# Kernel optimization log

Hardware: AMD Instinct MI355X
Metric: run time of the kernel (lower is better)

The kernel has to match this reference:

```python
import jax, jax.numpy as jnp
import numpy as np

F_, H_, W_ = 6, 16, 28          # latent video grid (frames, height, width)
DIM, NH = 1536, 12
HD = DIM // NH                   # 128
L = F_ * H_ * W_                 # 2688 tokens
EPS = 1e-6
BLOCK = 3 * H_ * W_              # block_causal_size = 3*frame_height*frame_width


def setup_inputs() -> dict:
    key = jax.random.key(0)
    ks = jax.random.split(key, 8)
    def lin(k):
        return jax.random.normal(k, (DIM, DIM), jnp.float32) * 0.02
    x = jax.random.normal(ks[0], (1, L, DIM), jnp.float32)
    # RoPE freqs: unit-modulus complex numbers stored as [...,(re,im)]
    ang = jax.random.uniform(ks[1], (1024, HD // 2), jnp.float32, -np.pi, np.pi)
    freqs = jnp.stack([jnp.cos(ang), jnp.sin(ang)], axis=-1)  # [1024, 64, 2]
    return {
        'x': x,
        'seq_lens': jnp.array([L], jnp.int32),
        'grid_sizes': jnp.array([[F_, H_, W_]], jnp.int32),
        'freqs': freqs,
        'Wq': lin(ks[2]), 'bq': jnp.zeros((DIM,), jnp.float32),
        'Wk': lin(ks[3]), 'bk': jnp.zeros((DIM,), jnp.float32),
        'Wv': lin(ks[4]), 'bv': jnp.zeros((DIM,), jnp.float32),
        'Wo': lin(ks[5]), 'bo': jnp.zeros((DIM,), jnp.float32),
        'gq': jnp.ones((DIM,), jnp.float32),
        'gk': jnp.ones((DIM,), jnp.float32),
    }


def _rmsnorm(x, g):
    # WanRMSNorm: x * rsqrt(mean(x^2) + eps) * weight
    return x * jax.lax.rsqrt(jnp.mean(x * x, axis=-1, keepdims=True) + EPS) * g


def _rope_apply(x, F, H, W, freqs, start_frame=0):
    # x: [B, L, n, d]; freqs: [1024, d//2, 2] (re, im). Per-axis split [c0, c3, c3].
    B, Lx, n, d = x.shape
    c = d // 2
    c3 = c // 3
    c0 = c - 2 * c3
    f0 = freqs[start_frame:start_frame + F, :c0]      # [F, c0, 2]
    f1 = freqs[:H, c0:c0 + c3]                        # [H, c3, 2]
    f2 = freqs[:W, c0 + c3:]                          # [W, c3, 2]
    ff = jnp.concatenate([
        jnp.broadcast_to(f0[:, None, None], (F, H, W, c0, 2)),
        jnp.broadcast_to(f1[None, :, None], (F, H, W, c3, 2)),
        jnp.broadcast_to(f2[None, None, :], (F, H, W, c3, 2)),
    ], axis=3).reshape(Lx, 1, c, 2)                   # [L, 1, c, 2]
    xr = x.reshape(B, Lx, n, c, 2)
    xre, xim = xr[..., 0], xr[..., 1]
    fre, fim = ff[None, ..., 0], ff[None, ..., 1]     # broadcast over batch, heads
    ore = xre * fre - xim * fim
    oim = xre * fim + xim * fre
    return jnp.stack([ore, oim], axis=-1).reshape(B, Lx, n, d)


def reference(x, seq_lens, grid_sizes, freqs, Wq, bq, Wk, bk, Wv, bv, Wo, bo, gq, gk):
    b, s = x.shape[:2]
    F = int(grid_sizes[0, 0]); H = int(grid_sizes[0, 1]); W = int(grid_sizes[0, 2])
    q = _rmsnorm(x @ Wq + bq, gq).reshape(b, s, NH, HD)
    k = _rmsnorm(x @ Wk + bk, gk).reshape(b, s, NH, HD)
    v = (x @ Wv + bv).reshape(b, s, NH, HD)
    rq = _rope_apply(q, F, H, W, freqs)
    rk = _rope_apply(k, F, H, W, freqs)
    # block-causal attention: query attends to keys in same-or-earlier 3-frame block
    scores = jnp.einsum('bihd,bjhd->bhij', rq, rk) * (HD ** -0.5)
    blk = jnp.arange(s) // (3 * H * W)
    mask = blk[None, :] <= blk[:, None]               # [s, s]
    scores = jnp.where(mask[None, None], scores, -1e30)
    attn = jax.nn.softmax(scores, axis=-1)
    out = jnp.einsum('bhij,bjhd->bihd', attn, v).reshape(b, s, DIM)
    return out @ Wo + bo
```

## Files before the change

kernel.cpp:

```cpp
#include <hip/hip_runtime.h>

#define L_SEQ 2688
#define DIM   1536
#define NH    12
#define HD    128
#define BLK_TOK 1344
#define HW_   448
#define W_    28
#define NKIT  24

typedef unsigned short u16;
typedef unsigned int   u32;
typedef __attribute__((ext_vector_type(4))) float f32x4;
typedef __attribute__((ext_vector_type(16))) float f32x16;
typedef __attribute__((ext_vector_type(8))) short s16x8;
typedef __attribute__((ext_vector_type(2))) int i32x2;
typedef __attribute__((ext_vector_type(4))) u32 u32x4;

__device__ __forceinline__ u16 f2b(float f) {
    u32 u = __builtin_bit_cast(u32, f);
    return (u16)((u + 0x7FFFu + ((u >> 16) & 1u)) >> 16);
}
__device__ __forceinline__ float b2f(u16 b) {
    return __builtin_bit_cast(float, (u32)b << 16);
}
__device__ __forceinline__ u32 cvt_pk_bf16(float lo, float hi) {
    u32 r;
    asm("v_cvt_pk_bf16_f32 %0, %1, %2" : "=v"(r) : "v"(lo), "v"(hi));
    return r;
}

__global__ __launch_bounds__(256) void k_prep(const float* __restrict__ x,
                                              u16* __restrict__ xb,
                                              const float* __restrict__ w0,
                                              const float* __restrict__ w1,
                                              const float* __restrict__ w2,
                                              const float* __restrict__ w3,
                                              u16* __restrict__ wt_all) {
    __shared__ float t[64][65];
    const int bid = blockIdx.x;
    if (bid < 2016) {
        const int n4 = (int)((size_t)L_SEQ * DIM / 4);
        int i = bid * 256 + threadIdx.x;
        const int stride = 2016 * 256;
        for (; i < n4; i += stride) {
            float4 v = ((const float4*)x)[i];
            ushort4 o;
            o.x = f2b(v.x); o.y = f2b(v.y); o.z = f2b(v.z); o.w = f2b(v.w);
            ((ushort4*)xb)[i] = o;
        }
    } else {
        const int idx = bid - 2016;
        const int z = idx / 576;
        const int rem = idx - z * 576;
        const int by = rem / 24, bx = rem - by * 24;
        const float* w = z == 0 ? w0 : z == 1 ? w1 : z == 2 ? w2 : w3;
        u16* wt = wt_all + (size_t)z * DIM * DIM;
        const int k0 = by * 64, n0 = bx * 64;
        const int c = threadIdx.x & 63, rg = threadIdx.x >> 6;
#pragma unroll
        for (int it = 0; it < 16; ++it) {
            int r = rg * 16 + it;
            t[r][c] = w[(size_t)(k0 + r) * DIM + n0 + c];
        }
        __syncthreads();
#pragma unroll
        for (int it = 0; it < 16; ++it) {
            int r = rg * 16 + it;
            wt[(size_t)(n0 + r) * DIM + k0 + c] = f2b(t[c][r]);
        }
    }
}

template<int OUTF>
__global__ __launch_bounds__(256) void k_gemm(const u16* __restrict__ A,
                                              const u16* __restrict__ Bt_all,
                                              const float* __restrict__ b0,
                                              const float* __restrict__ b1,
                                              const float* __restrict__ b2,
                                              void* __restrict__ out_all) {
    const int NW = OUTF ? 252 : 756;
    const int qc = NW >> 3, rq = NW & 7;
    const int xcd = blockIdx.x & 7, idx = blockIdx.x >> 3;
    const int work = (xcd < rq) ? xcd * (qc + 1) + idx
                                : rq * (qc + 1) + (xcd - rq) * qc + idx;
    int z, bm, bn;
    if (OUTF) { z = 0; bm = work / 12; bn = work - bm * 12; }
    else      { z = work / 252; int rem = work - z * 252; bm = rem / 12; bn = rem - bm * 12; }

    const u16* Bt = Bt_all + (size_t)z * DIM * DIM;
    const float* bias = z == 0 ? b0 : z == 1 ? b1 : b2;

    __shared__ u16 lbuf[2][2][8192];
    const int tid = threadIdx.x, lane = tid & 63, wid = tid >> 6;
    const int wm = wid >> 1, wn = wid & 1;
    const int q31 = lane & 31, hi = lane >> 5;

    const int sr = tid >> 3, sc = tid & 7;
    const int scol = 8 * (sc ^ (sr & 7));
    const u16* aRow = A  + (size_t)(bm * 128 + sr) * DIM + scol;
    const u16* bRow = Bt + (size_t)(bn * 128 + sr) * DIM + scol;

#define GSTAGE(KT, BUF)                                                            \
    {                                                                              \
        _Pragma("unroll")                                                          \
        for (int i = 0; i < 4; ++i)                                                \
            __builtin_amdgcn_global_load_lds(                                      \
                (const __attribute__((address_space(1))) u32*)(aRow + (size_t)i * 32 * DIM + (KT) * 64), \
                (__attribute__((address_space(3))) u32*)((char*)&lbuf[BUF][0][0] + i * 4096 + tid * 16), \
                16, 0, 0);                                                         \
        _Pragma("unroll")                                                          \
        for (int i = 0; i < 4; ++i)                                                \
            __builtin_amdgcn_global_load_lds(                                      \
                (const __attribute__((address_space(1))) u32*)(bRow + (size_t)i * 32 * DIM + (KT) * 64), \
                (__attribute__((address_space(3))) u32*)((char*)&lbuf[BUF][1][0] + i * 4096 + tid * 16), \
                16, 0, 0);                                                         \
    }

    f32x16 acc[2][2] = {};

    GSTAGE(0, 0);
    __syncthreads();
    for (int kt = 0; kt < NKIT; ++kt) {
        if (kt < NKIT - 1) GSTAGE(kt + 1, (kt + 1) & 1);
        const char* bufA = (const char*)&lbuf[kt & 1][0][0];
        const char* bufB = (const char*)&lbuf[kt & 1][1][0];
        s16x8 af[2][4], bf[2][4];
#pragma unroll
        for (int f = 0; f < 2; ++f)
#pragma unroll
            for (int kk = 0; kk < 4; ++kk) {
                const int ra = wm * 64 + f * 32 + q31;
                const int rb = wn * 64 + f * 32 + q31;
                const int cg = kk * 2 + hi;
                af[f][kk] = *(const s16x8*)(bufA + ra * 128 + (((cg) ^ (q31 & 7)) << 4));
                bf[f][kk] = *(const s16x8*)(bufB + rb * 128 + (((cg) ^ (q31 & 7)) << 4));
            }
        __builtin_amdgcn_s_setprio(1);
#pragma unroll
        for (int kk = 0; kk < 4; ++kk)
#pragma unroll
            for (int fm = 0; fm < 2; ++fm)
#pragma unroll
                for (int fn = 0; fn < 2; ++fn)
                    acc[fm][fn] = __builtin_amdgcn_mfma_f32_32x32x16_bf16(af[fm][kk], bf[fn][kk], acc[fm][fn], 0, 0, 0);
        __builtin_amdgcn_s_setprio(0);
        __syncthreads();
    }

#pragma unroll
    for (int fn = 0; fn < 2; ++fn) {
        const int col = bn * 128 + wn * 64 + fn * 32 + q31;
        const float bv = bias[col];
#pragma unroll
        for (int fm = 0; fm < 2; ++fm) {
#pragma unroll
            for (int e = 0; e < 16; ++e) {
                const int row = bm * 128 + wm * 64 + fm * 32 + (e & 3) + 8 * (e >> 2) + 4 * hi;
                const float v = acc[fm][fn][e] + bv;
                if (OUTF)
                    ((float*)out_all)[(size_t)row * DIM + col] = v;
                else
                    ((u16*)out_all)[(size_t)z * L_SEQ * DIM + (size_t)row * DIM + col] = f2b(v);
            }
        }
    }
#undef GSTAGE
}

__global__ __launch_bounds__(256) void k_post(const u16* __restrict__ pre_all,
                                              const float* __restrict__ gq,
                                              const float* __restrict__ gk,
                                              const float* __restrict__ freqs,
                                              u16* __restrict__ qh,
                                              u16* __restrict__ kh,
                                              u16* __restrict__ vt) {
    __shared__ float sred[4];
    __shared__ u16 tt[64][68];
    const int bid = blockIdx.x;
    const int t = threadIdx.x;
    if (bid < 5376) {
        const int which = bid & 1;
        const int i = bid >> 1;
        const u16* pre = pre_all + (size_t)which * L_SEQ * DIM;
        const float* g = which ? gk : gq;
        u16* outh = which ? kh : qh;
        const u32* prow = (const u32*)(pre + (size_t)i * DIM);

        float re[3], im[3];
        float ss = 0.f;
#pragma unroll
        for (int a = 0; a < 3; ++a) {
            u32 p = prow[t + a * 256];
            float x = b2f((u16)(p & 0xFFFFu)), y = b2f((u16)(p >> 16));
            re[a] = x; im[a] = y;
            ss += x * x + y * y;
        }
#pragma unroll
        for (int o = 32; o > 0; o >>= 1) ss += __shfl_down(ss, o, 64);
        if ((t & 63) == 0) sred[t >> 6] = ss;
        __syncthreads();
        float rms = rsqrtf((sred[0] + sred[1] + sred[2] + sred[3]) * (1.0f / DIM) + 1e-6f);

        const int f = i / HW_;
        const int rem = i - f * HW_;
        const int hp = rem / W_;
        const int wp = rem - hp * W_;
#pragma unroll
        for (int a = 0; a < 3; ++a) {
            int j = t + a * 256;
            int h = j >> 6, pj = j & 63;
            float2 gg = ((const float2*)g)[j];
            float x = re[a] * rms * gg.x;
            float y = im[a] * rms * gg.y;
            int ridx = pj < 22 ? f : (pj < 43 ? hp : wp);
            float2 cs = ((const float2*)freqs)[ridx * 64 + pj];
            float ore = x * cs.x - y * cs.y;
            float oim = x * cs.y + y * cs.x;
            u32 o = (u32)f2b(ore) | ((u32)f2b(oim) << 16);
            ((u32*)outh)[(size_t)h * (L_SEQ * 64) + (size_t)i * 64 + pj] = o;
        }
    } else {
        const int idx = bid - 5376;
        const int h = idx / 84;
        const int rem = idx - h * 84;
        const int d0 = (rem / 42) * 64, i0 = (rem % 42) * 64;
        const u16* vpre = pre_all + (size_t)2 * L_SEQ * DIM;
        const int c = t & 63, rg = t >> 6;
#pragma unroll
        for (int it = 0; it < 16; ++it) {
            int r = rg * 16 + it;
            tt[r][c] = vpre[(size_t)(i0 + r) * DIM + h * HD + d0 + c];
        }
        __syncthreads();
#pragma unroll
        for (int it = 0; it < 16; ++it) {
            int r = rg * 16 + it;
            vt[(size_t)h * (HD * L_SEQ) + (size_t)(d0 + r) * L_SEQ + i0 + c] = tt[c][r];
        }
    }
}

__global__ __launch_bounds__(256, 2) void k_attn(const u16* __restrict__ qh,
                                                 const u16* __restrict__ kh,
                                                 const u16* __restrict__ vt,
                                                 u16* __restrict__ ob,
                                                 float* __restrict__ Opart,
                                                 float* __restrict__ mlp) {
    __shared__ char lsm[2][32768];

    const int flat = blockIdx.x;
    const int xcd = flat & 7, idx = flat >> 3;
    const int work = (xcd < 4) ? (xcd * 95 + idx) : (380 + (xcd - 4) * 94 + idx);
    const int head = work / 63;
    const int bx = work - head * 63;
    int qt, kv0, mode;
    if (bx < 21)      { qt = bx;      kv0 = 0;  mode = 0; }
    else if (bx < 42) { qt = bx;      kv0 = 0;  mode = 1; }
    else              { qt = bx - 21; kv0 = 21; mode = 2; }

    const int tid = threadIdx.x, lane = tid & 63, w = tid >> 6;
    const int pairI = w >> 1;
    const int qhalf = w & 1;
    const int q31 = lane & 31, hi = lane >> 5;
    const size_t hOff = (size_t)head * ((size_t)L_SEQ * HD);
    const u16* Kh = kh + hOff;
    const u16* Vh = vt + hOff;
    const int qrow0 = qt * 64 + qhalf * 32;

    s16x8 aq[8];
#pragma unroll
    for (int kk = 0; kk < 8; ++kk)
        aq[kk] = *(const s16x8*)&qh[hOff + (size_t)(qrow0 + q31) * HD + kk * 16 + hi * 8];

    const int rh = tid >> 4, ck = tid & 15;
    const int rv = tid >> 3, cv = tid & 7;
    const int koff = 8 * (ck ^ rh);
    const int voff = 8 * (cv ^ (rv & 7));

#define STAGE_TILE(TG, BUF)                                                       \
    {                                                                             \
        char* dst = lsm[BUF];                                                     \
        _Pragma("unroll")                                                         \
        for (int i = 0; i < 4; ++i) {                                             \
            const u16* src = Kh + (size_t)((TG) * 64 + i * 16 + rh) * HD + koff;  \
            __builtin_amdgcn_global_load_lds(                                     \
                (const __attribute__((address_space(1))) u32*)src,                \
                (__attribute__((address_space(3))) u32*)(dst + i * 4096 + tid * 16), 16, 0, 0); \
        }                                                                         \
        _Pragma("unroll")                                                         \
        for (int i = 0; i < 4; ++i) {                                             \
            const u16* src = Vh + (size_t)(i * 32 + rv) * L_SEQ + (TG) * 64 + voff; \
            __builtin_amdgcn_global_load_lds(                                     \
                (const __attribute__((address_space(1))) u32*)src,                \
                (__attribute__((address_space(3))) u32*)(dst + 16384 + i * 4096 + tid * 16), 16, 0, 0); \
        }                                                                         \
    }

    f32x16 acc[4] = {};
    float mrun = -1e30f, lrun = 0.f;
    const float sc2 = 0.12751739646917983f;
    const int krow = pairI * 32 + q31;

    STAGE_TILE(kv0, 0);
    __syncthreads();
    for (int t = 0; t < 21; ++t) {
        if (t < 20) STAGE_TILE(kv0 + t + 1, (t + 1) & 1);
        const char* slot = lsm[t & 1];

        f32x16 sv0 = {}, sv1 = {};
        __builtin_amdgcn_s_setprio(1);
#pragma unroll
        for (int kk = 0; kk < 4; ++kk) {
            int off0 = krow * 256 + ((kk * 32 + hi * 16) ^ ((q31 & 15) << 4));
            int off1 = krow * 256 + (((kk + 4) * 32 + hi * 16) ^ ((q31 & 15) << 4));
            s16x8 kf0 = *(const s16x8*)(slot + off0);
            s16x8 kf1 = *(const s16x8*)(slot + off1);
            sv0 = __builtin_amdgcn_mfma_f32_32x32x16_bf16(kf0, aq[kk], sv0, 0, 0, 0);
            sv1 = __builtin_amdgcn_mfma_f32_32x32x16_bf16(kf1, aq[kk + 4], sv1, 0, 0, 0);
        }
        __builtin_amdgcn_s_setprio(0);
        f32x16 sv;
#pragma unroll
        for (int e = 0; e < 16; ++e) sv[e] = sv0[e] + sv1[e];

        float m8[8];
#pragma unroll
        for (int e = 0; e < 8; ++e) m8[e] = fmaxf(sv[e], sv[e + 8]);
        float m4a = fmaxf(m8[0], m8[1]), m4b = fmaxf(m8[2], m8[3]);
        float m4c = fmaxf(m8[4], m8[5]), m4d = fmaxf(m8[6], m8[7]);
        float mx = fmaxf(fmaxf(m4a, m4b), fmaxf(m4c, m4d));
        mx = fmaxf(mx, __shfl_xor(mx, 32, 64));
        mx *= sc2;
        const int resc = (mx - mrun) > 11.5f;
        const float mm = resc ? mx : mrun;
        const float fac = resc ? __builtin_amdgcn_exp2f(mrun - mm) : 1.0f;
        mrun = mm;
#pragma unroll
        for (int e = 0; e < 16; ++e)
            sv[e] = __builtin_amdgcn_exp2f(sv[e] * sc2 - mm);
        float s8[8];
#pragma unroll
        for (int e = 0; e < 8; ++e) s8[e] = sv[e] + sv[e + 8];
        float s4a = s8[0] + s8[1], s4b = s8[2] + s8[3];
        float s4c = s8[4] + s8[5], s4d = s8[6] + s8[7];
        float sum = (s4a + s4b) + (s4c + s4d);
        sum += __shfl_xor(sum, 32, 64);
        lrun = lrun * fac + sum;
        if (__any(resc)) {
#pragma unroll
            for (int ds = 0; ds < 4; ++ds)
#pragma unroll
                for (int e = 0; e < 16; ++e) acc[ds][e] *= fac;
        }

        s16x8 pa[2];
#pragma unroll
        for (int hf = 0; hf < 2; ++hf) {
            u32 a0 = cvt_pk_bf16(sv[hf * 8 + 0], sv[hf * 8 + 1]);
            u32 a1 = cvt_pk_bf16(sv[hf * 8 + 2], sv[hf * 8 + 3]);
            u32 b0 = cvt_pk_bf16(sv[hf * 8 + 4], sv[hf * 8 + 5]);
            u32 b1 = cvt_pk_bf16(sv[hf * 8 + 6], sv[hf * 8 + 7]);
            i32x2 r0 = __builtin_amdgcn_permlane32_swap((int)a0, (int)b0, false, false);
            i32x2 r1 = __builtin_amdgcn_permlane32_swap((int)a1, (int)b1, false, false);
            u32x4 fw;
            fw.x = (u32)r0.x; fw.y = (u32)r1.x; fw.z = (u32)r0.y; fw.w = (u32)r1.y;
            pa[hf] = __builtin_bit_cast(s16x8, fw);
        }

        __builtin_amdgcn_s_setprio(1);
#pragma unroll
        for (int jstep = 0; jstep < 2; ++jstep)
#pragma unroll
            for (int ds = 0; ds < 4; ++ds) {
                int off = 16384 + (ds * 32 + q31) * 128 +
                          ((pairI * 64 + jstep * 32 + hi * 16) ^ ((q31 & 7) << 4));
                s16x8 vf = *(const s16x8*)(slot + off);
                acc[ds] = __builtin_amdgcn_mfma_f32_32x32x16_bf16(vf, pa[jstep], acc[ds], 0, 0, 0);
            }
        __builtin_amdgcn_s_setprio(0);
        __syncthreads();
    }

    float2* mlb = (float2*)(lsm[1]);
    char* accb = lsm[0];
    if (w >= 2) {
        char* base = accb + qhalf * 16384 + lane * 256;
#pragma unroll
        for (int ds = 0; ds < 4; ++ds)
#pragma unroll
            for (int g = 0; g < 4; ++g) {
                f32x4 v4;
#pragma unroll
                for (int e = 0; e < 4; ++e) v4[e] = acc[ds][g * 4 + e];
                *(f32x4*)(base + (((ds * 4 + g) * 16) ^ ((lane & 15) << 4))) = v4;
            }
        if (hi == 0) {
            float2 t2; t2.x = mrun; t2.y = lrun;
            mlb[qhalf * 32 + q31] = t2;
        }
    }
    __syncthreads();
    if (w < 2) {
        float2 ml2 = mlb[qhalf * 32 + q31];
        float M = fmaxf(mrun, ml2.x);
        float wa = exp2f(mrun - M), wb = exp2f(ml2.x - M);
        lrun = lrun * wa + ml2.y * wb;
        mrun = M;
        const char* base = accb + qhalf * 16384 + lane * 256;
#pragma unroll
        for (int ds = 0; ds < 4; ++ds)
#pragma unroll
            for (int g = 0; g < 4; ++g) {
                f32x4 v4 = *(const f32x4*)(base + (((ds * 4 + g) * 16) ^ ((lane & 15) << 4)));
#pragma unroll
                for (int e = 0; e < 4; ++e) acc[ds][g * 4 + e] = acc[ds][g * 4 + e] * wa + v4[e] * wb;
            }
        if (mode == 0) {
            const float inv = 1.0f / lrun;
            u16* orow = ob + (size_t)(qrow0 + q31) * DIM + head * HD;
#pragma unroll
            for (int ds = 0; ds < 4; ++ds)
#pragma unroll
                for (int g = 0; g < 4; ++g) {
                    uint2 pk2;
                    pk2.x = cvt_pk_bf16(acc[ds][g * 4 + 0] * inv, acc[ds][g * 4 + 1] * inv);
                    pk2.y = cvt_pk_bf16(acc[ds][g * 4 + 2] * inv, acc[ds][g * 4 + 3] * inv);
                    *(uint2*)(orow + ds * 32 + g * 8 + hi * 4) = pk2;
                }
        } else {
            const int pairo = (head * 21 + (qt - 21)) * 2 + (mode - 1);
            float* Op = Opart + (size_t)pairo * (64 * 128);
            const int rowl = qhalf * 32 + q31;
#pragma unroll
            for (int ds = 0; ds < 4; ++ds)
#pragma unroll
                for (int g = 0; g < 4; ++g) {
                    float4 v4;
                    v4.x = acc[ds][g * 4 + 0]; v4.y = acc[ds][g * 4 + 1];
                    v4.z = acc[ds][g * 4 + 2]; v4.w = acc[ds][g * 4 + 3];
                    *(float4*)(&Op[rowl * 128 + ds * 32 + g * 8 + hi * 4]) = v4;
                }
            if (hi == 0) {
                float2 t2; t2.x = mrun; t2.y = lrun;
                ((float2*)mlp)[(size_t)pairo * 64 + rowl] = t2;
            }
        }
    }
#undef STAGE_TILE
}

__global__ __launch_bounds__(256) void k_merge(const float* __restrict__ Opart,
                                               const float* __restrict__ mlp,
                                               u16* __restrict__ ob) {
    const int b = blockIdx.x;
    const int qt2 = b % 21, head = b / 21;
    const int pair = head * 21 + qt2;
    const float* O0 = Opart + (size_t)pair * 2 * 8192;
    const float* O1 = O0 + 8192;
    const int tid = threadIdx.x;
    const int row = tid >> 2, cs = (tid & 3) * 32;
    float2 a = ((const float2*)mlp)[(size_t)pair * 2 * 64 + row];
    float2 c = ((const float2*)mlp)[(size_t)(pair * 2 + 1) * 64 + row];
    float M = fmaxf(a.x, c.x);
    float w0 = exp2f(a.x - M), w1 = exp2f(c.x - M);
    float inv = 1.0f / (w0 * a.y + w1 * c.y);
    w0 *= inv; w1 *= inv;
    const int rowg = BLK_TOK + qt2 * 64 + row;
    u32* orow = (u32*)(ob + (size_t)rowg * DIM + head * HD + cs);
    const float4* p0 = (const float4*)(O0 + row * 128 + cs);
    const float4* p1 = (const float4*)(O1 + row * 128 + cs);
#pragma unroll
    for (int u = 0; u < 8; ++u) {
        float4 x0 = p0[u], x1 = p1[u];
        float o0 = x0.x * w0 + x1.x * w1;
        float o1 = x0.y * w0 + x1.y * w1;
        float o2 = x0.z * w0 + x1.z * w1;
        float o3 = x0.w * w0 + x1.w * w1;
        orow[u * 2]     = (u32)f2b(o0) | ((u32)f2b(o1) << 16);
        orow[u * 2 + 1] = (u32)f2b(o2) | ((u32)f2b(o3) << 16);
    }
}

extern "C" void kernel_launch(void* const* d_in, const int* in_sizes, int n_in,
                              void* d_out, int out_size, void* d_ws, size_t ws_size,
                              hipStream_t stream) {
    const float* x     = (const float*)d_in[0];
    const float* freqs = (const float*)d_in[3];
    const float* Wq    = (const float*)d_in[4];
    const float* bq    = (const float*)d_in[5];
    const float* Wk    = (const float*)d_in[6];
    const float* bk    = (const float*)d_in[7];
    const float* Wv    = (const float*)d_in[8];
    const float* bv    = (const float*)d_in[9];
    const float* Wo    = (const float*)d_in[10];
    const float* bo    = (const float*)d_in[11];
    const float* gq    = (const float*)d_in[12];
    const float* gk    = (const float*)d_in[13];

    const size_t LD = (size_t)L_SEQ * DIM;
    u16* wt_all  = (u16*)d_ws;
    u16* xb      = wt_all + (size_t)4 * DIM * DIM;
    u16* pre_all = xb + LD;
    u16* qh      = pre_all + 3 * LD;
    u16* kh2     = qh + LD;
    u16* vt      = kh2 + LD;
    u16* ob      = vt + LD;
    float* Opart = (float*)pre_all;
    float* mlp   = Opart + (size_t)12 * 21 * 2 * 64 * 128;

    k_prep<<<dim3(2016 + 2304), 256, 0, stream>>>(x, xb, Wq, Wk, Wv, Wo, wt_all);
    k_gemm<0><<<dim3(756), 256, 0, stream>>>(xb, wt_all, bq, bk, bv, pre_all);
    k_post<<<dim3(5376 + 1008), 256, 0, stream>>>(pre_all, gq, gk, freqs, qh, kh2, vt);
    k_attn<<<dim3(756), 256, 0, stream>>>(qh, kh2, vt, ob, Opart, mlp);
    k_merge<<<dim3(252), 256, 0, stream>>>(Opart, mlp, ob);
    k_gemm<1><<<dim3(252), 256, 0, stream>>>(ob, wt_all + (size_t)3 * DIM * DIM, bo, bo, bo, d_out);
}
```

Before: 157.5 us.

## Drop split-KV attention and merge kernel; pair short and long query tiles

Attention no longer splits the second block's query tiles across two KV halves with a separate merge kernel. Each workgroup now processes a full query tile, running either 21 or 42 KV tiles, and the launch shrinks from 756 to 504 workgroups. Adjacent work indices alternate short and long tiles so each XCD gets a balanced mix. This removes the fp32 partial writes, the merge launch and its reads, at the cost of less parallelism and a longer critical path for the long tiles.

```diff
diff --git a/kernel.cpp b/kernel.cpp
--- a/kernel.cpp
+++ b/kernel.cpp
@@ -244,20 +244,16 @@
 __global__ __launch_bounds__(256, 2) void k_attn(const u16* __restrict__ qh,
                                                  const u16* __restrict__ kh,
                                                  const u16* __restrict__ vt,
-                                                 u16* __restrict__ ob,
-                                                 float* __restrict__ Opart,
-                                                 float* __restrict__ mlp) {
+                                                 u16* __restrict__ ob) {
     __shared__ char lsm[2][32768];
 
     const int flat = blockIdx.x;
     const int xcd = flat & 7, idx = flat >> 3;
-    const int work = (xcd < 4) ? (xcd * 95 + idx) : (380 + (xcd - 4) * 94 + idx);
-    const int head = work / 63;
-    const int bx = work - head * 63;
-    int qt, kv0, mode;
-    if (bx < 21)      { qt = bx;      kv0 = 0;  mode = 0; }
-    else if (bx < 42) { qt = bx;      kv0 = 0;  mode = 1; }
-    else              { qt = bx - 21; kv0 = 21; mode = 2; }
+    const int work = xcd * 63 + idx;
+    const int head = work / 42;
+    const int w2 = work - head * 42;
+    const int qt = (w2 & 1) ? 21 + (w2 >> 1) : (w2 >> 1);
+    const int nt = (qt < 21) ? 21 : 42;
 
     const int tid = threadIdx.x, lane = tid & 63, w = tid >> 6;
     const int pairI = w >> 1;
@@ -302,10 +298,10 @@
     const float sc2 = 0.12751739646917983f;
     const int krow = pairI * 32 + q31;
 
-    STAGE_TILE(kv0, 0);
+    STAGE_TILE(0, 0);
     __syncthreads();
-    for (int t = 0; t < 21; ++t) {
-        if (t < 20) STAGE_TILE(kv0 + t + 1, (t + 1) & 1);
+    for (int t = 0; t < nt; ++t) {
+        if (t < nt - 1) STAGE_TILE(t + 1, (t + 1) & 1);
         const char* slot = lsm[t & 1];
 
         f32x16 sv0 = {}, sv1 = {};
@@ -406,7 +402,6 @@
         float M = fmaxf(mrun, ml2.x);
         float wa = exp2f(mrun - M), wb = exp2f(ml2.x - M);
         lrun = lrun * wa + ml2.y * wb;
-        mrun = M;
         const char* base = accb + qhalf * 16384 + lane * 256;
 #pragma unroll
         for (int ds = 0; ds < 4; ++ds)
@@ -416,70 +411,19 @@
 #pragma unroll
                 for (int e = 0; e < 4; ++e) acc[ds][g * 4 + e] = acc[ds][g * 4 + e] * wa + v4[e] * wb;
             }
-        if (mode == 0) {
-            const float inv = 1.0f / lrun;
-            u16* orow = ob + (size_t)(qrow0 + q31) * DIM + head * HD;
-#pragma unroll
-            for (int ds = 0; ds < 4; ++ds)
-#pragma unroll
-                for (int g = 0; g < 4; ++g) {
-                    uint2 pk2;
-                    pk2.x = cvt_pk_bf16(acc[ds][g * 4 + 0] * inv, acc[ds][g * 4 + 1] * inv);
-                    pk2.y = cvt_pk_bf16(acc[ds][g * 4 + 2] * inv, acc[ds][g * 4 + 3] * inv);
-                    *(uint2*)(orow + ds * 32 + g * 8 + hi * 4) = pk2;
-                }
-        } else {
-            const int pairo = (head * 21 + (qt - 21)) * 2 + (mode - 1);
-            float* Op = Opart + (size_t)pairo * (64 * 128);
-            const int rowl = qhalf * 32 + q31;
-#pragma unroll
-            for (int ds = 0; ds < 4; ++ds)
-#pragma unroll
-                for (int g = 0; g < 4; ++g) {
-                    float4 v4;
-                    v4.x = acc[ds][g * 4 + 0]; v4.y = acc[ds][g * 4 + 1];
-                    v4.z = acc[ds][g * 4 + 2]; v4.w = acc[ds][g * 4 + 3];
-                    *(float4*)(&Op[rowl * 128 + ds * 32 + g * 8 + hi * 4]) = v4;
-                }
-            if (hi == 0) {
-                float2 t2; t2.x = mrun; t2.y = lrun;
-                ((float2*)mlp)[(size_t)pairo * 64 + rowl] = t2;
-            }
-        }
+        const float inv = 1.0f / lrun;
+        u16* orow = ob + (size_t)(qrow0 + q31) * DIM + head * HD;
+#pragma unroll
+        for (int ds = 0; ds < 4; ++ds)
+#pragma unroll
+            for (int g = 0; g < 4; ++g) {
+                uint2 pk2;
+                pk2.x = cvt_pk_bf16(acc[ds][g * 4 + 0] * inv, acc[ds][g * 4 + 1] * inv);
+                pk2.y = cvt_pk_bf16(acc[ds][g * 4 + 2] * inv, acc[ds][g * 4 + 3] * inv);
+                *(uint2*)(orow + ds * 32 + g * 8 + hi * 4) = pk2;
+            }
     }
 #undef STAGE_TILE
-}
-
-__global__ __launch_bounds__(256) void k_merge(const float* __restrict__ Opart,
-                                               const float* __restrict__ mlp,
-                                               u16* __restrict__ ob) {
-    const int b = blockIdx.x;
-    const int qt2 = b % 21, head = b / 21;
-    const int pair = head * 21 + qt2;
-    const float* O0 = Opart + (size_t)pair * 2 * 8192;
-    const float* O1 = O0 + 8192;
-    const int tid = threadIdx.x;
-    const int row = tid >> 2, cs = (tid & 3) * 32;
-    float2 a = ((const float2*)mlp)[(size_t)pair * 2 * 64 + row];
-    float2 c = ((const float2*)mlp)[(size_t)(pair * 2 + 1) * 64 + row];
-    float M = fmaxf(a.x, c.x);
-    float w0 = exp2f(a.x - M), w1 = exp2f(c.x - M);
-    float inv = 1.0f / (w0 * a.y + w1 * c.y);
-    w0 *= inv; w1 *= inv;
-    const int rowg = BLK_TOK + qt2 * 64 + row;
-    u32* orow = (u32*)(ob + (size_t)rowg * DIM + head * HD + cs);
-    const float4* p0 = (const float4*)(O0 + row * 128 + cs);
-    const float4* p1 = (const float4*)(O1 + row * 128 + cs);
-#pragma unroll
-    for (int u = 0; u < 8; ++u) {
-        float4 x0 = p0[u], x1 = p1[u];
-        float o0 = x0.x * w0 + x1.x * w1;
-        float o1 = x0.y * w0 + x1.y * w1;
-        float o2 = x0.z * w0 + x1.z * w1;
-        float o3 = x0.w * w0 + x1.w * w1;
-        orow[u * 2]     = (u32)f2b(o0) | ((u32)f2b(o1) << 16);
-        orow[u * 2 + 1] = (u32)f2b(o2) | ((u32)f2b(o3) << 16);
-    }
 }
 
 extern "C" void kernel_launch(void* const* d_in, const int* in_sizes, int n_in,
@@ -506,13 +450,10 @@
     u16* kh2     = qh + LD;
     u16* vt      = kh2 + LD;
     u16* ob      = vt + LD;
-    float* Opart = (float*)pre_all;
-    float* mlp   = Opart + (size_t)12 * 21 * 2 * 64 * 128;
 
     k_prep<<<dim3(2016 + 2304), 256, 0, stream>>>(x, xb, Wq, Wk, Wv, Wo, wt_all);
     k_gemm<0><<<dim3(756), 256, 0, stream>>>(xb, wt_all, bq, bk, bv, pre_all);
     k_post<<<dim3(5376 + 1008), 256, 0, stream>>>(pre_all, gq, gk, freqs, qh, kh2, vt);
-    k_attn<<<dim3(756), 256, 0, stream>>>(qh, kh2, vt, ob, Opart, mlp);
-    k_merge<<<dim3(252), 256, 0, stream>>>(Opart, mlp, ob);
+    k_attn<<<dim3(504), 256, 0, stream>>>(qh, kh2, vt, ob);
     k_gemm<1><<<dim3(252), 256, 0, stream>>>(ob, wt_all + (size_t)3 * DIM * DIM, bo, bo, bo, d_out);
 }
```

Result: faster. 154.4 us (-2.0%).
